# Performance work log

Measured on AMD Instinct MI355X. Metric: run time of the kernel, lower is better.

The kernel has to match this reference:

```python
import jax, jax.numpy as jnp
import numpy as np

K_NEIGHBORS = 32
TEMP = 0.5

def setup_inputs() -> dict:
    key = jax.random.key(0)
    k1, k2, k3 = jax.random.split(key, 3)
    B, D, N, F = 32, 256, 16384, 256
    query = jax.random.normal(k1, (B, D), dtype=jnp.float32)
    keys = jax.random.normal(k2, (B, D, N), dtype=jnp.float32)
    values = jax.random.normal(k3, (B, F, N), dtype=jnp.float32)
    return {"query": query, "keys": keys, "values": values}

def _compute_omega(s, k, t):
    # s: [..., N] similarities. Returns omega: [..., N, K]
    alpha0 = jax.nn.softmax(s, axis=-1)

    def step(alpha, _):
        om = jax.nn.softmax(alpha / t, axis=-1)
        alpha_new = alpha + jnp.log1p(-om)
        return alpha_new, om

    _, omegas = jax.lax.scan(step, alpha0, None, length=k)  # [K, ..., N]
    return jnp.moveaxis(omegas, 0, -1)  # [..., N, K]

def reference(query, keys, values):
    D = query.shape[-1]
    # sims: [..., N]; note the negative sign from the original module
    sims = -jnp.einsum('...d,...dn->...n', query, keys) / jnp.sqrt(jnp.float32(D))
    omega = _compute_omega(sims, K_NEIGHBORS, TEMP)  # [..., N, K]
    # weighted gather-sum: [..., K, F]
    k_nearest = jnp.einsum('...nk,...fn->...kf', omega, values)
    return k_nearest
```

## Files before the change

### kernel.cpp

```cpp
#include <hip/hip_runtime.h>
#include <hip/hip_bf16.h>

#define B_ 32
#define D_ 256
#define N_ 16384
#define F_ 256
#define K_ 32

#define NSPLIT 16
#define NSLICE (N_ / NSPLIT)

#define L2E 1.4426950408889634f

typedef __attribute__((ext_vector_type(8))) short bf16x8;
typedef __attribute__((ext_vector_type(4))) float f32x4;

__device__ __forceinline__ unsigned short f2bf(float x) {
    unsigned int u = __float_as_uint(x);
    u = (u + 0x7FFFu + ((u >> 16) & 1u)) >> 16;
    return (unsigned short)u;
}

__device__ __forceinline__ unsigned int pack_bf16(float x, float y) {
    unsigned int ux = __float_as_uint(x), uy = __float_as_uint(y);
    ux = (ux + 0x7FFFu + ((ux >> 16) & 1u)) >> 16;
    uy = (uy + 0x7FFFu + ((uy >> 16) & 1u)) & 0xFFFF0000u;
    return ux | uy;
}

__global__ __launch_bounds__(256) void sims_kernel(
    const float* __restrict__ q, const float* __restrict__ keys, float* __restrict__ sims)
{
    const int nt = N_ / 1024;
    int b = blockIdx.x / nt;
    int tile = blockIdx.x % nt;
    int n0 = tile * 1024 + threadIdx.x * 4;

    __shared__ float qs[D_];
    qs[threadIdx.x] = q[b * D_ + threadIdx.x];
    __syncthreads();

    const float* kb = keys + (size_t)b * D_ * N_ + n0;
    float ax = 0.f, ay = 0.f, az = 0.f, aw = 0.f;
    #pragma unroll 4
    for (int d = 0; d < D_; ++d) {
        float4 kv = *reinterpret_cast<const float4*>(kb + (size_t)d * N_);
        float qd = qs[d];
        ax = fmaf(qd, kv.x, ax); ay = fmaf(qd, kv.y, ay);
        az = fmaf(qd, kv.z, az); aw = fmaf(qd, kv.w, aw);
    }
    const float sc = -0.0625f;
    float4 o = make_float4(ax * sc, ay * sc, az * sc, aw * sc);
    *reinterpret_cast<float4*>(sims + b * N_ + n0) = o;
}

__device__ __forceinline__ float blk_max(float v, volatile float* red) {
    #pragma unroll
    for (int off = 32; off > 0; off >>= 1) v = fmaxf(v, __shfl_xor(v, off));
    if ((threadIdx.x & 63) == 0) red[threadIdx.x >> 6] = v;
    __syncthreads();
    if (threadIdx.x < 64) {
        float w = (threadIdx.x < 16) ? red[threadIdx.x] : -3.0e38f;
        #pragma unroll
        for (int off = 8; off > 0; off >>= 1) w = fmaxf(w, __shfl_xor(w, off));
        if (threadIdx.x == 0) red[16] = w;
    }
    __syncthreads();
    return red[16];
}
__device__ __forceinline__ float blk_sum(float v, volatile float* red) {
    #pragma unroll
    for (int off = 32; off > 0; off >>= 1) v += __shfl_xor(v, off);
    if ((threadIdx.x & 63) == 0) red[threadIdx.x >> 6] = v;
    __syncthreads();
    if (threadIdx.x < 64) {
        float w = (threadIdx.x < 16) ? red[threadIdx.x] : 0.0f;
        #pragma unroll
        for (int off = 8; off > 0; off >>= 1) w += __shfl_xor(w, off);
        if (threadIdx.x == 0) red[16] = w;
    }
    __syncthreads();
    return red[16];
}

__global__ __launch_bounds__(1024) void zeta_kernel(
    const float* __restrict__ sims, float* __restrict__ w0, float* __restrict__ izeta)
{
    int b = blockIdx.x, t = threadIdx.x;
    __shared__ float red1[17];
    __shared__ float red2[17];

    const float* sb = sims + (size_t)b * N_ + t * 16;
    float a[16];
    #pragma unroll
    for (int j = 0; j < 16; j += 4) {
        float4 v = *reinterpret_cast<const float4*>(sb + j);
        a[j] = v.x; a[j + 1] = v.y; a[j + 2] = v.z; a[j + 3] = v.w;
    }
    float m0 = -3.0e38f;
    #pragma unroll
    for (int j = 0; j < 16; ++j) m0 = fmaxf(m0, a[j]);
    m0 = blk_max(m0, red1);

    float zs = 0.f;
    #pragma unroll
    for (int j = 0; j < 16; ++j) {
        a[j] = __builtin_amdgcn_exp2f((a[j] - m0) * L2E);
        zs += a[j];
    }
    float Z = blk_sum(zs, red2);
    float c2 = 2.0f * L2E / Z;
    #pragma unroll
    for (int j = 0; j < 16; ++j) a[j] = __builtin_amdgcn_exp2f(a[j] * c2);

    float* wp = w0 + (size_t)b * N_ + t * 16;
    #pragma unroll
    for (int j = 0; j < 16; j += 4)
        *reinterpret_cast<float4*>(wp + j) = make_float4(a[j], a[j+1], a[j+2], a[j+3]);

    for (int k = 0; k < K_; ++k) {
        float zz = 0.f;
        #pragma unroll
        for (int j = 0; j < 16; ++j) zz += a[j];
        float Zk = blk_sum(zz, red2);
        float izk = 1.0f / Zk;
        if (t == 0) izeta[b * K_ + k] = izk;
        #pragma unroll
        for (int j = 0; j < 16; ++j) {
            float u = 1.0f - a[j] * izk;
            a[j] *= u * u;
        }
    }
}

__global__ __launch_bounds__(256) void pv_kernel(
    const float* __restrict__ values, const float* __restrict__ w0,
    const float* __restrict__ izeta, float* __restrict__ part)
{
    int ns = blockIdx.x % NSPLIT;
    int b  = blockIdx.x / NSPLIT;
    int t = threadIdx.x;

    __shared__ unsigned char om_lds[K_ * 2048];

    int n0 = ns * NSLICE;

    {
        float4 u4 = *reinterpret_cast<const float4*>(w0 + (size_t)b * N_ + n0 + t * 4);
        float u[4] = {u4.x, u4.y, u4.z, u4.w};
        const float* zb = izeta + b * K_;
        int colbyte = t * 8;
        #pragma unroll 8
        for (int k = 0; k < K_; ++k) {
            float izk = zb[k];
            float om0 = u[0] * izk, om1 = u[1] * izk;
            float om2 = u[2] * izk, om3 = u[3] * izk;
            unsigned int lo = pack_bf16(om0, om1);
            unsigned int hi = pack_bf16(om2, om3);
            int addr = (k * 2048 + colbyte) ^ ((k & 7) << 4);
            *reinterpret_cast<uint2*>(&om_lds[addr]) = make_uint2(lo, hi);
            float a0 = 1.f - om0, a1 = 1.f - om1, a2 = 1.f - om2, a3 = 1.f - om3;
            u[0] *= a0 * a0; u[1] *= a1 * a1; u[2] *= a2 * a2; u[3] *= a3 * a3;
        }
    }
    __syncthreads();

    int wv = t >> 6;
    int l  = t & 63;
    int lr = l & 15;
    int lq = l >> 4;
    int fbase = wv * 64;

    const float* vb = values + (size_t)b * F_ * N_;

    f32x4 acc[4][2];
    #pragma unroll
    for (int ti = 0; ti < 4; ++ti)
        #pragma unroll
        for (int kt = 0; kt < 2; ++kt)
            acc[ti][kt] = (f32x4){0.f, 0.f, 0.f, 0.f};

    for (int nb = 0; nb < NSLICE; nb += 32) {
        int cb = (nb + lq * 8) * 2;
        int xr = (lr & 7) << 4;
        bf16x8 a0 = *reinterpret_cast<const bf16x8*>(&om_lds[(lr * 2048 + cb) ^ xr]);
        bf16x8 a1 = *reinterpret_cast<const bf16x8*>(&om_lds[((lr + 16) * 2048 + cb) ^ xr]);
        #pragma unroll
        for (int ti = 0; ti < 4; ++ti) {
            const float* vp = vb + (size_t)(fbase + ti * 16 + lr) * N_ + n0 + nb + lq * 8;
            float4 x0 = *reinterpret_cast<const float4*>(vp);
            float4 x1 = *reinterpret_cast<const float4*>(vp + 4);
            union { unsigned short s[8]; bf16x8 v; } bv;
            bv.s[0] = f2bf(x0.x); bv.s[1] = f2bf(x0.y);
            bv.s[2] = f2bf(x0.z); bv.s[3] = f2bf(x0.w);
            bv.s[4] = f2bf(x1.x); bv.s[5] = f2bf(x1.y);
            bv.s[6] = f2bf(x1.z); bv.s[7] = f2bf(x1.w);
            acc[ti][0] = __builtin_amdgcn_mfma_f32_16x16x32_bf16(a0, bv.v, acc[ti][0], 0, 0, 0);
            acc[ti][1] = __builtin_amdgcn_mfma_f32_16x16x32_bf16(a1, bv.v, acc[ti][1], 0, 0, 0);
        }
    }

    float* pb = part + ((size_t)(b * NSPLIT + ns) * K_) * F_;
    #pragma unroll
    for (int ti = 0; ti < 4; ++ti) {
        int f = fbase + ti * 16 + lr;
        #pragma unroll
        for (int kt = 0; kt < 2; ++kt) {
            #pragma unroll
            for (int r = 0; r < 4; ++r) {
                int k = kt * 16 + lq * 4 + r;
                pb[(size_t)k * F_ + f] = acc[ti][kt][r];
            }
        }
    }
}

__global__ __launch_bounds__(256) void reduce_kernel(
    const float* __restrict__ part, float* __restrict__ out)
{
    int idx = (blockIdx.x * 256 + threadIdx.x) * 4;
    int f = idx % F_;
    int bk = idx / F_;
    int k = bk % K_;
    int b = bk / K_;
    const float* p = part + (((size_t)b * NSPLIT) * K_ + k) * F_ + f;
    float4 s = make_float4(0.f, 0.f, 0.f, 0.f);
    #pragma unroll 4
    for (int ns = 0; ns < NSPLIT; ++ns) {
        float4 v = *reinterpret_cast<const float4*>(p + (size_t)ns * K_ * F_);
        s.x += v.x; s.y += v.y; s.z += v.z; s.w += v.w;
    }
    *reinterpret_cast<float4*>(out + idx) = s;
}

extern "C" void kernel_launch(void* const* d_in, const int* in_sizes, int n_in,
                              void* d_out, int out_size, void* d_ws, size_t ws_size,
                              hipStream_t stream)
{
    const float* q      = (const float*)d_in[0];
    const float* keys   = (const float*)d_in[1];
    const float* values = (const float*)d_in[2];
    float* out = (float*)d_out;

    char* ws = (char*)d_ws;
    float* sims  = (float*)ws;
    float* w0    = (float*)(ws + (size_t)B_ * N_ * 4);
    float* izeta = (float*)(ws + (size_t)2 * B_ * N_ * 4);
    float* part  = (float*)(ws + (size_t)2 * B_ * N_ * 4 + 4096);

    sims_kernel  <<<B_ * (N_ / 1024), 256, 0, stream>>>(q, keys, sims);
    zeta_kernel  <<<B_, 1024, 0, stream>>>(sims, w0, izeta);
    pv_kernel    <<<B_ * NSPLIT, 256, 0, stream>>>(values, w0, izeta, part);
    reduce_kernel<<<(B_ * K_ * F_) / 1024, 256, 0, stream>>>(part, out);
}
```

Before: 271.5 us.

## Double N-split in pv kernel, shrink LDS, and cut zeta reduction barriers

The pv stage now splits each batch's N dimension into twice as many slices, halving the per-block omega LDS footprint, and adds an occupancy hint so more blocks can be resident to hide the values stream latency. The zeta kernel's per-iteration block reduction is replaced by a single-barrier scheme that double-buffers the partial sums, so every thread sums all 16 wave partials instead of paying two barriers per iteration. The sims loop unroll is also raised. The cost is twice the partial-sum traffic into the reduce kernel, whose loop now covers 32 slices.

New measurement: 251.1 us, median of 2. -7.5%, faster.

```diff
diff --git a/kernel.cpp b/kernel.cpp
--- a/kernel.cpp
+++ b/kernel.cpp
@@ -7,7 +7,7 @@
 #define F_ 256
 #define K_ 32
 
-#define NSPLIT 16
+#define NSPLIT 32
 #define NSLICE (N_ / NSPLIT)
 
 #define L2E 1.4426950408889634f
@@ -42,7 +42,7 @@
 
     const float* kb = keys + (size_t)b * D_ * N_ + n0;
     float ax = 0.f, ay = 0.f, az = 0.f, aw = 0.f;
-    #pragma unroll 4
+    #pragma unroll 8
     for (int d = 0; d < D_; ++d) {
         float4 kv = *reinterpret_cast<const float4*>(kb + (size_t)d * N_);
         float qd = qs[d];
@@ -88,7 +88,8 @@
 {
     int b = blockIdx.x, t = threadIdx.x;
     __shared__ float red1[17];
-    __shared__ float red2[17];
+    __shared__ float redA[16];
+    __shared__ float redB[16];
 
     const float* sb = sims + (size_t)b * N_ + t * 16;
     float a[16];
@@ -108,7 +109,7 @@
         a[j] = __builtin_amdgcn_exp2f((a[j] - m0) * L2E);
         zs += a[j];
     }
-    float Z = blk_sum(zs, red2);
+    float Z = blk_sum(zs, red1);
     float c2 = 2.0f * L2E / Z;
     #pragma unroll
     for (int j = 0; j < 16; ++j) a[j] = __builtin_amdgcn_exp2f(a[j] * c2);
@@ -117,12 +118,23 @@
     #pragma unroll
     for (int j = 0; j < 16; j += 4)
         *reinterpret_cast<float4*>(wp + j) = make_float4(a[j], a[j+1], a[j+2], a[j+3]);
+    __syncthreads();
 
     for (int k = 0; k < K_; ++k) {
         float zz = 0.f;
         #pragma unroll
         for (int j = 0; j < 16; ++j) zz += a[j];
-        float Zk = blk_sum(zz, red2);
+        #pragma unroll
+        for (int off = 32; off > 0; off >>= 1) zz += __shfl_xor(zz, off);
+        float* buf = (k & 1) ? redB : redA;
+        if ((t & 63) == 0) buf[t >> 6] = zz;
+        __syncthreads();
+        float4 p0 = *reinterpret_cast<float4*>(&buf[0]);
+        float4 p1 = *reinterpret_cast<float4*>(&buf[4]);
+        float4 p2 = *reinterpret_cast<float4*>(&buf[8]);
+        float4 p3 = *reinterpret_cast<float4*>(&buf[12]);
+        float Zk = ((p0.x + p0.y) + (p0.z + p0.w)) + ((p1.x + p1.y) + (p1.z + p1.w))
+                 + ((p2.x + p2.y) + (p2.z + p2.w)) + ((p3.x + p3.y) + (p3.z + p3.w));
         float izk = 1.0f / Zk;
         if (t == 0) izeta[b * K_ + k] = izk;
         #pragma unroll
@@ -133,7 +145,7 @@
     }
 }
 
-__global__ __launch_bounds__(256) void pv_kernel(
+__global__ __launch_bounds__(256, 4) void pv_kernel(
     const float* __restrict__ values, const float* __restrict__ w0,
     const float* __restrict__ izeta, float* __restrict__ part)
 {
@@ -141,26 +153,23 @@
     int b  = blockIdx.x / NSPLIT;
     int t = threadIdx.x;
 
-    __shared__ unsigned char om_lds[K_ * 2048];
+    __shared__ unsigned char om_lds[K_ * NSLICE * 2];
 
     int n0 = ns * NSLICE;
 
     {
-        float4 u4 = *reinterpret_cast<const float4*>(w0 + (size_t)b * N_ + n0 + t * 4);
-        float u[4] = {u4.x, u4.y, u4.z, u4.w};
+        float2 u2 = *reinterpret_cast<const float2*>(w0 + (size_t)b * N_ + n0 + t * 2);
+        float u0 = u2.x, u1 = u2.y;
         const float* zb = izeta + b * K_;
-        int colbyte = t * 8;
+        int colbyte = t * 4;
         #pragma unroll 8
         for (int k = 0; k < K_; ++k) {
             float izk = zb[k];
-            float om0 = u[0] * izk, om1 = u[1] * izk;
-            float om2 = u[2] * izk, om3 = u[3] * izk;
-            unsigned int lo = pack_bf16(om0, om1);
-            unsigned int hi = pack_bf16(om2, om3);
-            int addr = (k * 2048 + colbyte) ^ ((k & 7) << 4);
-            *reinterpret_cast<uint2*>(&om_lds[addr]) = make_uint2(lo, hi);
-            float a0 = 1.f - om0, a1 = 1.f - om1, a2 = 1.f - om2, a3 = 1.f - om3;
-            u[0] *= a0 * a0; u[1] *= a1 * a1; u[2] *= a2 * a2; u[3] *= a3 * a3;
+            float om0 = u0 * izk, om1 = u1 * izk;
+            int addr = (k * 1024 + colbyte) ^ ((k & 7) << 4);
+            *reinterpret_cast<unsigned int*>(&om_lds[addr]) = pack_bf16(om0, om1);
+            float a0 = 1.f - om0, a1 = 1.f - om1;
+            u0 *= a0 * a0; u1 *= a1 * a1;
         }
     }
     __syncthreads();
@@ -180,11 +189,12 @@
         for (int kt = 0; kt < 2; ++kt)
             acc[ti][kt] = (f32x4){0.f, 0.f, 0.f, 0.f};
 
+    int xr = (lr & 7) << 4;
+
     for (int nb = 0; nb < NSLICE; nb += 32) {
         int cb = (nb + lq * 8) * 2;
-        int xr = (lr & 7) << 4;
-        bf16x8 a0 = *reinterpret_cast<const bf16x8*>(&om_lds[(lr * 2048 + cb) ^ xr]);
-        bf16x8 a1 = *reinterpret_cast<const bf16x8*>(&om_lds[((lr + 16) * 2048 + cb) ^ xr]);
+        bf16x8 a0 = *reinterpret_cast<const bf16x8*>(&om_lds[(lr * 1024 + cb) ^ xr]);
+        bf16x8 a1 = *reinterpret_cast<const bf16x8*>(&om_lds[((lr + 16) * 1024 + cb) ^ xr]);
         #pragma unroll
         for (int ti = 0; ti < 4; ++ti) {
             const float* vp = vb + (size_t)(fbase + ti * 16 + lr) * N_ + n0 + nb + lq * 8;
```
